# Kernel tuning notes

Hardware: AMD Instinct MI355X
Metric: run time of the kernel (lower is better)

## Reference

```python
import jax, jax.numpy as jnp
import numpy as np
import math

INPUT_DIM = 256
HIDDEN_DIM = 128
N = 8192
GATE_TEMPERATURE = 1.0
LN_EPS = 1e-5


def setup_inputs() -> dict:
    key = jax.random.key(0)
    ks = jax.random.split(key, 10)
    s_in = 1.0 / math.sqrt(INPUT_DIM)
    s_h = 1.0 / math.sqrt(HIDDEN_DIM)
    s_cat = 1.0 / math.sqrt(INPUT_DIM + HIDDEN_DIM)
    return {
        "node_features": jax.random.normal(ks[0], (N, INPUT_DIM), jnp.float32),
        "adj_matrix": jax.random.uniform(ks[1], (N, N), jnp.float32),
        "msg_w": jax.random.uniform(ks[2], (INPUT_DIM, HIDDEN_DIM), jnp.float32, -s_in, s_in),
        "msg_b": jax.random.uniform(ks[3], (HIDDEN_DIM,), jnp.float32, -s_in, s_in),
        "upd_w": jax.random.uniform(ks[4], (INPUT_DIM + HIDDEN_DIM, HIDDEN_DIM), jnp.float32, -s_cat, s_cat),
        "upd_b": jax.random.uniform(ks[5], (HIDDEN_DIM,), jnp.float32, -s_cat, s_cat),
        "gate_q_w": jax.random.uniform(ks[6], (HIDDEN_DIM, HIDDEN_DIM), jnp.float32, -s_h, s_h),
        "gate_k_w": jax.random.uniform(ks[7], (HIDDEN_DIM, HIDDEN_DIM), jnp.float32, -s_h, s_h),
        "gate_bias": jnp.float32(-1.0),
        "ln_gamma": jnp.ones((HIDDEN_DIM,), jnp.float32),
        "ln_beta": jnp.zeros((HIDDEN_DIM,), jnp.float32),
    }


def reference(node_features, adj_matrix, msg_w, msg_b, upd_w, upd_b,
              gate_q_w, gate_k_w, gate_bias, ln_gamma, ln_beta):
    # messages: [N, hidden]
    messages = node_features @ msg_w + msg_b
    # edge gates: sigmoid(QK^T / (sqrt(d)*tau) + b), masked by adjacency
    q = messages @ gate_q_w  # [N, hidden]
    k = messages @ gate_k_w  # [N, hidden]
    scale = 1.0 / (math.sqrt(HIDDEN_DIM) * max(GATE_TEMPERATURE, 1e-6))
    scores = (q @ k.T) * scale  # [N, N]
    gates_masked = jax.nn.sigmoid(scores + gate_bias) * adj_matrix
    aggregated = gates_masked @ messages  # [N, hidden]
    combined = jnp.concatenate([node_features, aggregated], axis=1)
    updated = jax.nn.relu(combined @ upd_w + upd_b)
    # LayerNorm over last dim
    mu = jnp.mean(updated, axis=-1, keepdims=True)
    var = jnp.var(updated, axis=-1, keepdims=True)
    normed = (updated - mu) * jax.lax.rsqrt(var + LN_EPS)
    return normed * ln_gamma + ln_beta
```

## Files before the change

kernel.cpp:

```cpp
#include <hip/hip_runtime.h>
#include <hip/hip_bf16.h>
#include <stdint.h>

#define NN 8192
#define DIN 256
#define HID 128
#define SCALE 0.08838834764831845f

typedef __attribute__((ext_vector_type(8))) short short8;
typedef __attribute__((ext_vector_type(4))) float f32x4;
typedef __attribute__((ext_vector_type(16))) float f32x16;
typedef __attribute__((ext_vector_type(8))) unsigned short u16x8;
typedef __attribute__((ext_vector_type(4))) unsigned short u16x4;
typedef __attribute__((ext_vector_type(4))) unsigned int u32x4;

__device__ __forceinline__ unsigned short f2bf(float f) {
  unsigned int u = __builtin_bit_cast(unsigned int, f);
  u += 0x7FFFu + ((u >> 16) & 1u);
  return (unsigned short)(u >> 16);
}

__device__ __forceinline__ unsigned int cvtpk(float lo, float hi) {
  unsigned int r;
  asm("v_cvt_pk_bf16_f32 %0, %1, %2" : "=v"(r) : "v"(lo), "v"(hi));
  return r;
}

__device__ __forceinline__ void async16(const void* g, void* l) {
  __builtin_amdgcn_global_load_lds(
      (const __attribute__((address_space(1))) unsigned int*)g,
      (__attribute__((address_space(3))) unsigned int*)l, 16, 0, 0);
}

__global__ __launch_bounds__(256) void kw0(
    const float* __restrict__ msg_w, const float* __restrict__ qw,
    const float* __restrict__ kw, const float* __restrict__ upd_w,
    unsigned short* __restrict__ mwT, unsigned short* __restrict__ qwT,
    unsigned short* __restrict__ kwT, unsigned short* __restrict__ w_t) {
  int idx0 = blockIdx.x * 1792 + threadIdx.x;
#pragma unroll
  for (int it = 0; it < 7; ++it) {
    int idx = idx0 + it * 256;
    if (idx < 32768) {
      int h = idx >> 8, j = idx & 255;
      mwT[idx] = f2bf(msg_w[j * HID + h]);
    } else if (idx < 49152) {
      int r = idx - 32768, h = r >> 7, j = r & 127;
      qwT[r] = f2bf(qw[j * HID + h]);
    } else if (idx < 65536) {
      int r = idx - 49152, h = r >> 7, j = r & 127;
      kwT[r] = f2bf(kw[j * HID + h]);
    } else {
      int r = idx - 65536, h = r / 384, j = r % 384;
      w_t[r] = f2bf(upd_w[j * HID + h]);
    }
  }
}

__global__ __launch_bounds__(256) void ka(
    const float* __restrict__ nf, const unsigned short* __restrict__ mwT,
    const float* __restrict__ msg_b, const unsigned short* __restrict__ qwT,
    const unsigned short* __restrict__ kwT, unsigned short* __restrict__ q_bf,
    unsigned short* __restrict__ k_bf, unsigned short* __restrict__ m_t,
    unsigned short* __restrict__ nf_bf) {
  __shared__ __align__(16) unsigned short nfl[32][264];
  __shared__ __align__(16) unsigned short ml[32][136];
  int t = threadIdx.x, l = t & 63, w = t >> 6;
  int lr = l & 15, lg = l >> 4;
  int i0 = blockIdx.x * 32;
  {
    int row = t >> 3, c0 = (t & 7) * 32;
    const float* src = nf + (size_t)(i0 + row) * DIN + c0;
    unsigned short* gdst = nf_bf + (size_t)(i0 + row) * DIN + c0;
#pragma unroll
    for (int v = 0; v < 4; ++v) {
      f32x4 a = *(const f32x4*)(src + v * 8);
      f32x4 b = *(const f32x4*)(src + v * 8 + 4);
      u16x8 o;
#pragma unroll
      for (int e = 0; e < 4; ++e) { o[e] = f2bf(a[e]); o[4 + e] = f2bf(b[e]); }
      *(u16x8*)&nfl[row][c0 + v * 8] = o;
      *(u16x8*)(gdst + v * 8) = o;
    }
  }
  __syncthreads();
  int rl = (w >> 1) * 16;
  int nb = (w & 1) * 4;
  f32x4 macc[4];
#pragma unroll
  for (int nt = 0; nt < 4; ++nt) macc[nt] = (f32x4){0.f, 0.f, 0.f, 0.f};
#pragma unroll
  for (int kk = 0; kk < 8; ++kk) {
    short8 af = *(const short8*)&nfl[rl + lr][kk * 32 + lg * 8];
#pragma unroll
    for (int nt = 0; nt < 4; ++nt) {
      short8 bf = *(const short8*)(mwT + (size_t)((nb + nt) * 16 + lr) * DIN + kk * 32 + lg * 8);
      macc[nt] = __builtin_amdgcn_mfma_f32_16x16x32_bf16(af, bf, macc[nt], 0, 0, 0);
    }
  }
#pragma unroll
  for (int nt = 0; nt < 4; ++nt) {
    int col = (nb + nt) * 16 + lr;
    float bias = msg_b[col];
#pragma unroll
    for (int reg = 0; reg < 4; ++reg)
      ml[rl + lg * 4 + reg][col] = f2bf(macc[nt][reg] + bias);
  }
  __syncthreads();
  {
    int hh = t >> 1, i8 = (t & 1) * 16;
    u16x8 o0, o1;
#pragma unroll
    for (int v = 0; v < 8; ++v) { o0[v] = ml[i8 + v][hh]; o1[v] = ml[i8 + 8 + v][hh]; }
    *(u16x8*)(m_t + (size_t)hh * NN + i0 + i8) = o0;
    *(u16x8*)(m_t + (size_t)hh * NN + i0 + i8 + 8) = o1;
  }
  f32x4 qacc[4], kacc[4];
#pragma unroll
  for (int nt = 0; nt < 4; ++nt) {
    qacc[nt] = (f32x4){0.f, 0.f, 0.f, 0.f};
    kacc[nt] = (f32x4){0.f, 0.f, 0.f, 0.f};
  }
#pragma unroll
  for (int kk = 0; kk < 4; ++kk) {
    short8 af = *(const short8*)&ml[rl + lr][kk * 32 + lg * 8];
#pragma unroll
    for (int nt = 0; nt < 4; ++nt) {
      short8 bq = *(const short8*)(qwT + (size_t)((nb + nt) * 16 + lr) * HID + kk * 32 + lg * 8);
      short8 bk = *(const short8*)(kwT + (size_t)((nb + nt) * 16 + lr) * HID + kk * 32 + lg * 8);
      qacc[nt] = __builtin_amdgcn_mfma_f32_16x16x32_bf16(af, bq, qacc[nt], 0, 0, 0);
      kacc[nt] = __builtin_amdgcn_mfma_f32_16x16x32_bf16(af, bk, kacc[nt], 0, 0, 0);
    }
  }
#pragma unroll
  for (int nt = 0; nt < 4; ++nt) {
    int col = (nb + nt) * 16 + lr;
#pragma unroll
    for (int reg = 0; reg < 4; ++reg) {
      int row = i0 + rl + lg * 4 + reg;
      q_bf[(size_t)row * HID + col] = f2bf(qacc[nt][reg]);
      k_bf[(size_t)row * HID + col] = f2bf(kacc[nt][reg]);
    }
  }
}

__global__ __launch_bounds__(256, 3) void kb(
    const unsigned short* __restrict__ q_bf, const unsigned short* __restrict__ k_bf,
    const unsigned short* __restrict__ m_t, const float* __restrict__ adj,
    const float* __restrict__ gate_bias, float* __restrict__ agg_parts) {
  __shared__ __align__(16) char klds[16384];
  __shared__ __align__(16) char mlds[16384];
  int t = threadIdx.x, l = t & 63, w = t >> 6;
  int li = l & 31, hi = l >> 5;
  int lin = blockIdx.x + blockIdx.y * 64;
  int nlin = (lin & 7) * 128 + (lin >> 3);
  int bx = nlin & 63, by = nlin >> 6;
  int i0 = bx * 128;
  int jbase = by * 512;
  float gb = gate_bias[0];

  int irow = i0 + w * 32 + li;
  short8 qf[8];
#pragma unroll
  for (int kc16 = 0; kc16 < 8; ++kc16)
    qf[kc16] = *(const short8*)(q_bf + (size_t)irow * HID + kc16 * 16 + hi * 8);

  const float* arow = adj + (size_t)irow * NN;

  int krow = t >> 4;
  int klb = (t & 15) ^ (krow & 7);
  int mrow = t >> 3;
  int mlb = (t & 7) ^ (mrow & 7);

  f32x16 acc[4];
#pragma unroll
  for (int ht = 0; ht < 4; ++ht)
#pragma unroll
    for (int r = 0; r < 16; ++r) acc[ht][r] = 0.f;

  for (int jt = 0; jt < 8; ++jt) {
    int j0 = jbase + jt * 64;
    __syncthreads();
    f32x4 adjv[8];
#pragma unroll
    for (int q2 = 0; q2 < 8; ++q2)
      adjv[q2] = *(const f32x4*)(arow + j0 + (q2 >> 2) * 32 + (q2 & 3) * 8 + hi * 4);
#pragma unroll
    for (int p = 0; p < 4; ++p)
      async16(k_bf + (size_t)(j0 + p * 16 + krow) * HID + klb * 8,
              klds + p * 4096 + w * 1024);
#pragma unroll
    for (int p = 0; p < 4; ++p)
      async16(m_t + (size_t)(p * 32 + mrow) * NN + j0 + mlb * 8,
              mlds + p * 4096 + w * 1024);
    __syncthreads();

#pragma unroll
    for (int jt32 = 0; jt32 < 2; ++jt32) {
      int j32 = jt32 * 32;
      int jrow = j32 + li;
      f32x16 s;
#pragma unroll
      for (int r = 0; r < 16; ++r) s[r] = 0.f;
#pragma unroll
      for (int kc16 = 0; kc16 < 8; ++kc16) {
        const short8 kf = *(const short8*)(
            klds + jrow * 256 + (((kc16 * 2 + hi) ^ (jrow & 7)) * 16));
        s = __builtin_amdgcn_mfma_f32_32x32x16_bf16(kf, qf[kc16], s, 0, 0, 0);
      }
      float g[16];
#pragma unroll
      for (int r = 0; r < 16; ++r) {
        float x = fmaf(s[r], SCALE, gb);
        float e = __expf(-x);
        g[r] = adjv[jt32 * 4 + (r >> 2)][r & 3] * __builtin_amdgcn_rcpf(1.0f + e);
      }
#pragma unroll
      for (int kc = 0; kc < 2; ++kc) {
        unsigned int r0 = cvtpk(g[kc * 8 + 0], g[kc * 8 + 1]);
        unsigned int r1 = cvtpk(g[kc * 8 + 2], g[kc * 8 + 3]);
        unsigned int r2 = cvtpk(g[kc * 8 + 4], g[kc * 8 + 5]);
        unsigned int r3 = cvtpk(g[kc * 8 + 6], g[kc * 8 + 7]);
        asm volatile("v_permlane32_swap_b32 %0, %1" : "+v"(r0), "+v"(r2));
        asm volatile("v_permlane32_swap_b32 %0, %1" : "+v"(r1), "+v"(r3));
        const short8 gf = __builtin_bit_cast(short8, (u32x4){r0, r1, r2, r3});
        int slot = jt32 * 4 + kc * 2 + hi;
#pragma unroll
        for (int ht = 0; ht < 4; ++ht) {
          int h = ht * 32 + li;
          const short8 mf = *(const short8*)(
              mlds + h * 128 + ((slot ^ (h & 7)) * 16));
          acc[ht] = __builtin_amdgcn_mfma_f32_32x32x16_bf16(mf, gf, acc[ht], 0, 0, 0);
        }
      }
    }
  }
  float* part = agg_parts + (size_t)by * HID * NN;
#pragma unroll
  for (int ht = 0; ht < 4; ++ht)
#pragma unroll
    for (int r = 0; r < 16; ++r) {
      int h = ht * 32 + (r & 3) + 8 * (r >> 2) + 4 * hi;
      part[(size_t)h * NN + i0 + w * 32 + li] = acc[ht][r];
    }
}

__global__ __launch_bounds__(256) void kc(
    const unsigned short* __restrict__ nf_bf, const float* __restrict__ agg_parts,
    const unsigned short* __restrict__ w_t, const float* __restrict__ upd_b,
    const float* __restrict__ gamma, const float* __restrict__ beta,
    float* __restrict__ out) {
  __shared__ __align__(16) unsigned short aggl[64][136];
  int t = threadIdx.x, l = t & 63, w = t >> 6;
  int i0 = blockIdx.x * 64;
  {
    const size_t ps = (size_t)HID * NN;
#pragma unroll
    for (int pass = 0; pass < 8; ++pass) {
      int h = pass * 16 + (t >> 4);
      const float* pb = agg_parts + (size_t)h * NN + i0 + (t & 15) * 4;
      f32x4 s = (f32x4){0.f, 0.f, 0.f, 0.f};
#pragma unroll
      for (int c = 0; c < 16; ++c) s += *(const f32x4*)(pb + c * ps);
#pragma unroll
      for (int e = 0; e < 4; ++e) aggl[(t & 15) * 4 + e][h] = f2bf(s[e]);
    }
  }
  __syncthreads();
  int lr = l & 15, lg = l >> 4;
  int arow = i0 + w * 16 + lr;
  short8 af[12];
#pragma unroll
  for (int kk = 0; kk < 8; ++kk)
    af[kk] = *(const short8*)(nf_bf + (size_t)arow * DIN + kk * 32 + lg * 8);
#pragma unroll
  for (int kk = 8; kk < 12; ++kk)
    af[kk] = *(const short8*)(&aggl[w * 16 + lr][(kk - 8) * 32 + lg * 8]);
  f32x4 acc[8];
#pragma unroll
  for (int nt = 0; nt < 8; ++nt) acc[nt] = (f32x4){0.f, 0.f, 0.f, 0.f};
#pragma unroll
  for (int kk = 0; kk < 12; ++kk)
#pragma unroll
    for (int nt = 0; nt < 8; ++nt) {
      const short8 bf =
          *(const short8*)(w_t + (size_t)(nt * 16 + lr) * 384 + kk * 32 + lg * 8);
      acc[nt] = __builtin_amdgcn_mfma_f32_16x16x32_bf16(af[kk], bf, acc[nt], 0, 0, 0);
    }
  float ub[8], ga[8], be[8];
#pragma unroll
  for (int nt = 0; nt < 8; ++nt) {
    ub[nt] = upd_b[nt * 16 + lr];
    ga[nt] = gamma[nt * 16 + lr];
    be[nt] = beta[nt * 16 + lr];
  }
  float v[8][4], sum[4], sq[4];
#pragma unroll
  for (int reg = 0; reg < 4; ++reg) { sum[reg] = 0.f; sq[reg] = 0.f; }
#pragma unroll
  for (int nt = 0; nt < 8; ++nt)
#pragma unroll
    for (int reg = 0; reg < 4; ++reg) {
      float x = acc[nt][reg] + ub[nt];
      x = fmaxf(x, 0.f);
      v[nt][reg] = x;
      sum[reg] += x;
      sq[reg] = fmaf(x, x, sq[reg]);
    }
#pragma unroll
  for (int reg = 0; reg < 4; ++reg) {
#pragma unroll
    for (int m = 1; m < 16; m <<= 1) {
      sum[reg] += __shfl_xor(sum[reg], m, 16);
      sq[reg] += __shfl_xor(sq[reg], m, 16);
    }
  }
#pragma unroll
  for (int reg = 0; reg < 4; ++reg) {
    float mu = sum[reg] * (1.0f / 128.0f);
    float var = sq[reg] * (1.0f / 128.0f) - mu * mu;
    float rstd = rsqrtf(var + 1e-5f);
    int orow = i0 + w * 16 + lg * 4 + reg;
#pragma unroll
    for (int nt = 0; nt < 8; ++nt) {
      float y = (v[nt][reg] - mu) * rstd * ga[nt] + be[nt];
      out[(size_t)orow * HID + nt * 16 + lr] = y;
    }
  }
}

extern "C" void kernel_launch(void* const* d_in, const int* in_sizes, int n_in,
                              void* d_out, int out_size, void* d_ws, size_t ws_size,
                              hipStream_t stream) {
  const float* nf    = (const float*)d_in[0];
  const float* adj   = (const float*)d_in[1];
  const float* msg_w = (const float*)d_in[2];
  const float* msg_b = (const float*)d_in[3];
  const float* upd_w = (const float*)d_in[4];
  const float* upd_b = (const float*)d_in[5];
  const float* qw    = (const float*)d_in[6];
  const float* kw    = (const float*)d_in[7];
  const float* gbias = (const float*)d_in[8];
  const float* gamma = (const float*)d_in[9];
  const float* beta  = (const float*)d_in[10];
  char* ws = (char*)d_ws;
  unsigned short* q_bf  = (unsigned short*)(ws);
  unsigned short* k_bf  = (unsigned short*)(ws + 0x200000);
  unsigned short* m_t   = (unsigned short*)(ws + 0x400000);
  unsigned short* nf_bf = (unsigned short*)(ws + 0x600000);
  unsigned short* w_t   = (unsigned short*)(ws + 0xA00000);
  unsigned short* mwT   = (unsigned short*)(ws + 0xA20000);
  unsigned short* qwT   = (unsigned short*)(ws + 0xA30000);
  unsigned short* kwT   = (unsigned short*)(ws + 0xA38000);
  float* agg            = (float*)(ws + 0xA40000);

  kw0<<<64, 256, 0, stream>>>(msg_w, qw, kw, upd_w, mwT, qwT, kwT, w_t);
  ka<<<256, 256, 0, stream>>>(nf, mwT, msg_b, qwT, kwT, q_bf, k_bf, m_t, nf_bf);
  kb<<<dim3(64, 16), 256, 0, stream>>>(q_bf, k_bf, m_t, adj, gbias, agg);
  kc<<<128, 256, 0, stream>>>(nf_bf, agg, w_t, upd_b, gamma, beta, (float*)d_out);
}
```

Before: 147.5 us.

## Pre-tile K and transposed messages into MFMA fragment order for linear LDS loads

The producer kernel now writes k_bf and m_t in a blocked layout that matches the MFMA operand fragment order, so the gating kernel can copy contiguous 4KB chunks into LDS with linear addresses. Each lane then reads its fragment at a fixed offset of lane*16, with no XOR swizzle arithmetic. The aim is fully coalesced global-to-LDS copies, conflict-free LDS reads and less address math in the inner loop. In exchange the intermediate layouts become specialised and tied to these exact tile shapes.

```diff
diff --git a/kernel.cpp b/kernel.cpp
--- a/kernel.cpp
+++ b/kernel.cpp
@@ -11,7 +11,6 @@
 typedef __attribute__((ext_vector_type(4))) float f32x4;
 typedef __attribute__((ext_vector_type(16))) float f32x16;
 typedef __attribute__((ext_vector_type(8))) unsigned short u16x8;
-typedef __attribute__((ext_vector_type(4))) unsigned short u16x4;
 typedef __attribute__((ext_vector_type(4))) unsigned int u32x4;
 
 __device__ __forceinline__ unsigned short f2bf(float f) {
@@ -108,12 +107,19 @@
   }
   __syncthreads();
   {
-    int hh = t >> 1, i8 = (t & 1) * 16;
+    int hh = t >> 1;
+    int Ibase = (t & 1) * 16;
+    int I = i0 + Ibase;
+    unsigned short* mb =
+        m_t + ((size_t)(I >> 4) * 4 + (hh >> 5)) * 512 + (hh & 31) * 8;
     u16x8 o0, o1;
 #pragma unroll
-    for (int v = 0; v < 8; ++v) { o0[v] = ml[i8 + v][hh]; o1[v] = ml[i8 + 8 + v][hh]; }
-    *(u16x8*)(m_t + (size_t)hh * NN + i0 + i8) = o0;
-    *(u16x8*)(m_t + (size_t)hh * NN + i0 + i8 + 8) = o1;
+    for (int v = 0; v < 8; ++v) {
+      o0[v] = ml[Ibase + v][hh];
+      o1[v] = ml[Ibase + 8 + v][hh];
+    }
+    *(u16x8*)(mb) = o0;
+    *(u16x8*)(mb + 256) = o1;
   }
   f32x4 qacc[4], kacc[4];
 #pragma unroll
@@ -139,7 +145,9 @@
     for (int reg = 0; reg < 4; ++reg) {
       int row = i0 + rl + lg * 4 + reg;
       q_bf[(size_t)row * HID + col] = f2bf(qacc[nt][reg]);
-      k_bf[(size_t)row * HID + col] = f2bf(kacc[nt][reg]);
+      size_t ko = ((size_t)(row >> 5) * 8 + (col >> 4)) * 512 +
+                  (((col >> 3) & 1) * 32 + (row & 31)) * 8 + (col & 7);
+      k_bf[ko] = f2bf(kacc[nt][reg]);
     }
   }
 }
@@ -167,10 +175,8 @@
 
   const float* arow = adj + (size_t)irow * NN;
 
-  int krow = t >> 4;
-  int klb = (t & 15) ^ (krow & 7);
-  int mrow = t >> 3;
-  int mlb = (t & 7) ^ (mrow & 7);
+  const char* kread = klds + l * 16;
+  const char* mread = mlds + l * 16;
 
   f32x16 acc[4];
 #pragma unroll
@@ -185,27 +191,26 @@
 #pragma unroll
     for (int q2 = 0; q2 < 8; ++q2)
       adjv[q2] = *(const f32x4*)(arow + j0 + (q2 >> 2) * 32 + (q2 & 3) * 8 + hi * 4);
-#pragma unroll
-    for (int p = 0; p < 4; ++p)
-      async16(k_bf + (size_t)(j0 + p * 16 + krow) * HID + klb * 8,
-              klds + p * 4096 + w * 1024);
-#pragma unroll
-    for (int p = 0; p < 4; ++p)
-      async16(m_t + (size_t)(p * 32 + mrow) * NN + j0 + mlb * 8,
-              mlds + p * 4096 + w * 1024);
+    {
+      const unsigned short* ksrc = k_bf + (size_t)j0 * 128;
+      const unsigned short* msrc = m_t + (size_t)j0 * 128;
+#pragma unroll
+      for (int p = 0; p < 4; ++p)
+        async16(ksrc + p * 2048 + t * 8, klds + p * 4096 + w * 1024);
+#pragma unroll
+      for (int p = 0; p < 4; ++p)
+        async16(msrc + p * 2048 + t * 8, mlds + p * 4096 + w * 1024);
+    }
     __syncthreads();
 
 #pragma unroll
     for (int jt32 = 0; jt32 < 2; ++jt32) {
-      int j32 = jt32 * 32;
-      int jrow = j32 + li;
       f32x16 s;
 #pragma unroll
       for (int r = 0; r < 16; ++r) s[r] = 0.f;
 #pragma unroll
       for (int kc16 = 0; kc16 < 8; ++kc16) {
-        const short8 kf = *(const short8*)(
-            klds + jrow * 256 + (((kc16 * 2 + hi) ^ (jrow & 7)) * 16));
+        const short8 kf = *(const short8*)(kread + jt32 * 8192 + kc16 * 1024);
         s = __builtin_amdgcn_mfma_f32_32x32x16_bf16(kf, qf[kc16], s, 0, 0, 0);
       }
       float g[16];
@@ -224,12 +229,10 @@
         asm volatile("v_permlane32_swap_b32 %0, %1" : "+v"(r0), "+v"(r2));
         asm volatile("v_permlane32_swap_b32 %0, %1" : "+v"(r1), "+v"(r3));
         const short8 gf = __builtin_bit_cast(short8, (u32x4){r0, r1, r2, r3});
-        int slot = jt32 * 4 + kc * 2 + hi;
+        int jblk = (jt32 * 2 + kc) * 4096;
 #pragma unroll
         for (int ht = 0; ht < 4; ++ht) {
-          int h = ht * 32 + li;
-          const short8 mf = *(const short8*)(
-              mlds + h * 128 + ((slot ^ (h & 7)) * 16));
+          const short8 mf = *(const short8*)(mread + jblk + ht * 1024);
           acc[ht] = __builtin_amdgcn_mfma_f32_32x32x16_bf16(mf, gf, acc[ht], 0, 0, 0);
         }
       }
```

Result: faster. 135.2 us (-8.4%).
